# Performance work log

Measured on AMD Instinct MI355X. Metric: run time of the kernel, lower is better.

## Reference

```python
import jax, jax.numpy as jnp
import numpy as np

EPS = 1e-6
BETA = 0.25
COMMIT_W = 1.0


def setup_inputs() -> dict:
    key = jax.random.key(0)
    k1, k2, k3 = jax.random.split(key, 3)
    b, c, h, w = 8, 256, 32, 32
    n_e, e_dim = 16384, 256
    z = jax.random.normal(k1, (b, c, h, w), jnp.float32)
    # frozen_codebook = randn(n_e, e_dim) * e_dim**-0.5
    codebook = jax.random.normal(k2, (n_e, e_dim), jnp.float32) * (e_dim ** -0.5)
    # nn.Linear(e_dim, in_channels, bias=False) weight: (in_channels, e_dim)
    W = jax.random.normal(k3, (c, e_dim), jnp.float32) * (e_dim ** -0.5)
    return {"z": z, "codebook": codebook, "W": W}


def _rotate_to(src, tgt):
    # Rotation trick (Fifty et al.): rotate src onto tgt direction with a
    # detached Householder-style transform; gradient flows through src only.
    # src, tgt: (n, d)
    norm_src = jnp.linalg.norm(src, axis=-1, keepdims=True)
    norm_tgt = jnp.linalg.norm(tgt, axis=-1, keepdims=True)
    u = src / (norm_src + EPS)
    q = tgt / (norm_tgt + EPS)
    uq = u + q
    w_ = jax.lax.stop_gradient(uq / (jnp.linalg.norm(uq, axis=-1, keepdims=True) + EPS))
    u_d = jax.lax.stop_gradient(u)
    q_d = jax.lax.stop_gradient(q)
    rot = (src
           - 2.0 * jnp.sum(src * w_, axis=-1, keepdims=True) * w_
           + 2.0 * jnp.sum(src * u_d, axis=-1, keepdims=True) * q_d)
    return rot * jax.lax.stop_gradient(norm_tgt / (norm_src + EPS))


def reference(z, codebook, W):
    b, c, h, w = z.shape
    # b c h w -> (b*h*w, c)
    z_flat = jnp.transpose(z, (0, 2, 3, 1)).reshape(-1, c)
    # implicit codebook: frozen codes through linear projection
    emb = codebook @ W.T  # (n_e, c)
    # squared L2 distances (no grad needed for argmin)
    d = (jnp.sum(z_flat ** 2, axis=1, keepdims=True)
         + jnp.sum(emb ** 2, axis=1)
         - 2.0 * (z_flat @ emb.T))  # (n_tok, n_e)
    indices = jnp.argmin(d, axis=1)  # (n_tok,)
    z_q_flat = emb[indices]  # gather quantized vectors
    loss = COMMIT_W * (jnp.mean((jax.lax.stop_gradient(z_flat) - z_q_flat) ** 2)
                       + BETA * jnp.mean((z_flat - jax.lax.stop_gradient(z_q_flat)) ** 2))
    z_q_flat = _rotate_to(z_flat, z_q_flat)
    z_q = jnp.transpose(z_q_flat.reshape(b, h, w, c), (0, 3, 1, 2))
    return z_q, loss, indices
```

## Files before the change

kernel.cpp:

```cpp
#include <hip/hip_runtime.h>
#include <math.h>

#define EPSV 1e-6f
#define NTOK 8192
#define NE   16384
#define DIM  256

using short8 = __attribute__((ext_vector_type(8))) short;
using f32x4v = __attribute__((ext_vector_type(4))) float;
using f32x16 = __attribute__((ext_vector_type(16))) float;

__device__ __forceinline__ unsigned short f2bf(float v) {
    unsigned int u = __float_as_uint(v);
    u += 0x7fffu + ((u >> 16) & 1u);
    return (unsigned short)(u >> 16);
}
__device__ __forceinline__ float bf2f(unsigned short h) {
    return __uint_as_float(((unsigned int)h) << 16);
}

__device__ __forceinline__ void gload_lds16(const void* g, void* s) {
    __builtin_amdgcn_global_load_lds(
        (const __attribute__((address_space(1))) void*)g,
        (__attribute__((address_space(3))) void*)s, 16, 0, 0);
}

__device__ __forceinline__ void split8(const float4 a, const float4 b,
                                       short8& h, short8& l) {
    float f[8] = {a.x, a.y, a.z, a.w, b.x, b.y, b.z, b.w};
#pragma unroll
    for (int j = 0; j < 8; ++j) {
        unsigned short hh = f2bf(f[j]);
        h[j] = (short)hh;
        l[j] = (short)f2bf(f[j] - bf2f(hh));
    }
}

__global__ __launch_bounds__(256) void k0a_transpose(
    const float* __restrict__ zin, float* __restrict__ z_flat,
    unsigned short* __restrict__ zh, unsigned short* __restrict__ zl) {
    __shared__ float tile[64][65];
    const int tid = threadIdx.x;
    const int yx0 = blockIdx.x * 64, c0 = blockIdx.y * 64, b = blockIdx.z;
    const int sub = tid >> 6, ln = tid & 63;
#pragma unroll
    for (int j = 0; j < 16; ++j) {
        int cl = j * 4 + sub;
        tile[cl][ln] = zin[((size_t)(b * 256 + c0 + cl) << 10) + yx0 + ln];
    }
    __syncthreads();
#pragma unroll
    for (int j = 0; j < 16; ++j) {
        int tl = j * 4 + sub;
        float v = tile[ln][tl];
        size_t o = (size_t)(b * 1024 + yx0 + tl) * 256 + c0 + ln;
        z_flat[o] = v;
        unsigned short h = f2bf(v);
        zh[o] = h;
        zl[o] = f2bf(v - bf2f(h));
    }
}

__global__ __launch_bounds__(256) void k0b_sz(const float* __restrict__ z_flat,
                                              float* __restrict__ sz) {
    const int w = threadIdx.x >> 6, lane = threadIdx.x & 63;
    const int t = blockIdx.x * 4 + w;
    const float4 v = *(const float4*)(z_flat + (size_t)t * 256 + lane * 4);
    double s = (double)v.x * v.x + (double)v.y * v.y + (double)v.z * v.z +
               (double)v.w * v.w;
#pragma unroll
    for (int m = 1; m < 64; m <<= 1) s += __shfl_xor(s, m);
    if (lane == 0) sz[t] = (float)s;
}

__global__ __launch_bounds__(256) void k0pre(const float* __restrict__ Wm,
                                             unsigned short* __restrict__ wh,
                                             unsigned short* __restrict__ wl) {
    const int i = (blockIdx.x * 256 + threadIdx.x) * 4;
    const float4 v = *(const float4*)(Wm + i);
    float f[4] = {v.x, v.y, v.z, v.w};
#pragma unroll
    for (int j = 0; j < 4; ++j) {
        unsigned short h = f2bf(f[j]);
        wh[i + j] = h;
        wl[i + j] = f2bf(f[j] - bf2f(h));
    }
}

__global__ __launch_bounds__(256, 2) void k0c_emb(
    const float* __restrict__ cb, const unsigned short* __restrict__ wh,
    const unsigned short* __restrict__ wl, float* __restrict__ emb,
    unsigned short* __restrict__ eh, unsigned short* __restrict__ el) {
    __shared__ char smemC[65536];
    const int tid = threadIdx.x;
    const int w = tid >> 6, lane = tid & 63;
    const int quad = lane >> 4, lr = lane & 15;
    const int wr = w & 1, wc = w >> 1;
    const int n0 = blockIdx.x * 128, c0 = blockIdx.y * 128;

    f32x4v acc[4][4];
#pragma unroll
    for (int mt = 0; mt < 4; ++mt)
#pragma unroll
        for (int nt = 0; nt < 4; ++nt)
            acc[mt][nt] = (f32x4v){0.f, 0.f, 0.f, 0.f};

    for (int kc = 0; kc < 4; ++kc) {
        __syncthreads();
#pragma unroll
        for (int i = 0; i < 16; ++i) {
            int s = i * 4 + w;
            int u = s * 64 + lane;
            const void* g;
            if (s < 32) {
                int kg = u >> 7, row = u & 127;
                g = cb + (size_t)(n0 + row) * 256 + kc * 64 + kg * 4;
            } else if (s < 48) {
                int u1 = u - 2048;
                int kg = u1 >> 7, row = u1 & 127;
                g = wh + (size_t)(c0 + row) * 256 + kc * 64 + kg * 8;
            } else {
                int u2 = u - 3072;
                int kg = u2 >> 7, row = u2 & 127;
                g = wl + (size_t)(c0 + row) * 256 + kc * 64 + kg * 8;
            }
            gload_lds16(g, smemC + ((size_t)u << 4));
        }
        __syncthreads();
#pragma unroll
        for (int ks = 0; ks < 2; ++ks) {
            short8 Ah[4], Al[4], Bh[4], Bl[4];
#pragma unroll
            for (int mt = 0; mt < 4; ++mt) {
                int m = wr * 64 + mt * 16 + lr;
                int kg2 = ks * 8 + quad * 2;
                float4 f0 = *(const float4*)(smemC + (((size_t)kg2 * 128 + m) << 4));
                float4 f1 = *(const float4*)(smemC + ((((size_t)kg2 + 1) * 128 + m) << 4));
                split8(f0, f1, Ah[mt], Al[mt]);
            }
#pragma unroll
            for (int nt = 0; nt < 4; ++nt) {
                int n = wc * 64 + nt * 16 + lr;
                int ku = (ks * 4 + quad) * 128 + n;
                Bh[nt] = *(const short8*)(smemC + (((size_t)2048 + ku) << 4));
                Bl[nt] = *(const short8*)(smemC + (((size_t)3072 + ku) << 4));
            }
#pragma unroll
            for (int mt = 0; mt < 4; ++mt)
#pragma unroll
                for (int nt = 0; nt < 4; ++nt) {
                    f32x4v a = acc[mt][nt];
                    a = __builtin_amdgcn_mfma_f32_16x16x32_bf16(Ah[mt], Bh[nt], a, 0, 0, 0);
                    a = __builtin_amdgcn_mfma_f32_16x16x32_bf16(Ah[mt], Bl[nt], a, 0, 0, 0);
                    a = __builtin_amdgcn_mfma_f32_16x16x32_bf16(Al[mt], Bh[nt], a, 0, 0, 0);
                    a = __builtin_amdgcn_mfma_f32_16x16x32_bf16(Al[mt], Bl[nt], a, 0, 0, 0);
                    acc[mt][nt] = a;
                }
        }
    }
#pragma unroll
    for (int mt = 0; mt < 4; ++mt)
#pragma unroll
        for (int rr = 0; rr < 4; ++rr) {
            int row = n0 + wr * 64 + mt * 16 + quad * 4 + rr;
#pragma unroll
            for (int nt = 0; nt < 4; ++nt) {
                int col = c0 + wc * 64 + nt * 16 + lr;
                size_t o = (size_t)row * 256 + col;
                float v = acc[mt][nt][rr];
                emb[o] = v;
                unsigned short h = f2bf(v);
                eh[o] = h;
                el[o] = f2bf(v - bf2f(h));
            }
        }
}

__global__ __launch_bounds__(256) void k0d_se(const float* __restrict__ emb,
                                              float* __restrict__ se) {
    const int w = threadIdx.x >> 6, lane = threadIdx.x & 63;
    const int n = blockIdx.x * 4 + w;
    const float4 v = *(const float4*)(emb + (size_t)n * 256 + lane * 4);
    double s = (double)v.x * v.x + (double)v.y * v.y + (double)v.z * v.z +
               (double)v.w * v.w;
#pragma unroll
    for (int m = 1; m < 64; m <<= 1) s += __shfl_xor(s, m);
    if (lane == 0) se[n] = (float)s;
}

__global__ __launch_bounds__(256, 2) void k1_dist_argmin(
    const unsigned short* __restrict__ zh, const unsigned short* __restrict__ zl,
    const unsigned short* __restrict__ eh, const unsigned short* __restrict__ el,
    const float* __restrict__ sz, const float* __restrict__ se,
    float* __restrict__ pval, int* __restrict__ pidx) {
    __shared__ char smem[65536];
    const int tid = threadIdx.x;
    const int w = tid >> 6, lane = tid & 63;
    const int col = lane & 31, half = lane >> 5;
    const int tokBase = blockIdx.x * 128;
    const int rowBase = tokBase + w * 32;
    const int slab = blockIdx.y;
    const int slabBase = slab * 2048;

    short8 Ah[16], Al[16];
#pragma unroll
    for (int ks = 0; ks < 16; ++ks) {
        size_t o = (size_t)(rowBase + col) * 256 + ks * 16 + half * 8;
        Ah[ks] = *(const short8*)(zh + o);
        Al[ks] = *(const short8*)(zl + o);
    }

    float szrow[16];
#pragma unroll
    for (int r = 0; r < 16; ++r)
        szrow[r] = sz[rowBase + (r & 3) + 8 * (r >> 2) + 4 * half];

    float minv[16];
    int mini[16];
#pragma unroll
    for (int r = 0; r < 16; ++r) {
        minv[r] = INFINITY;
        mini[r] = 0;
    }

    const int BASE = col * 512 + ((half ^ (col & 1)) << 4) + ((col & 30) << 4);

    auto stage = [&](int buf, int ch) {
        const int colBase = slabBase + ch * 32;
#pragma unroll
        for (int i = 0; i < 8; ++i) {
            int u = i * 256 + tid;
            int fmt = u >> 10;
            int u1 = u & 1023;
            int c2 = u1 >> 5, kgs = u1 & 31;
            int kg = kgs ^ c2;
            const unsigned short* g =
                (fmt ? el : eh) + (size_t)(colBase + c2) * 256 + kg * 8;
            gload_lds16(g, smem + buf * 32768 + ((size_t)u << 4));
        }
    };

    stage(0, 0);
    __syncthreads();

    for (int ch = 0; ch < 64; ++ch) {
        const int cur = ch & 1;
        if (ch + 1 < 64) stage(cur ^ 1, ch + 1);

        const float sec = se[slabBase + ch * 32 + col];

        f32x16 acc = {};
        const char* sp = smem + cur * 32768;
        const char* spl = sp + 16384;
#pragma unroll
        for (int ks = 0; ks < 16; ++ks) {
            const int a = BASE ^ (ks << 5);
            short8 Bh = *(const short8*)(sp + a);
            short8 Bl = *(const short8*)(spl + a);
            acc = __builtin_amdgcn_mfma_f32_32x32x16_bf16(Ah[ks], Bh, acc, 0, 0, 0);
            acc = __builtin_amdgcn_mfma_f32_32x32x16_bf16(Ah[ks], Bl, acc, 0, 0, 0);
            acc = __builtin_amdgcn_mfma_f32_32x32x16_bf16(Al[ks], Bh, acc, 0, 0, 0);
        }

        const int colg = slabBase + ch * 32 + col;
#pragma unroll
        for (int r = 0; r < 16; ++r) {
            float szse = __fadd_rn(szrow[r], sec);
            float d = fmaf(-2.0f, acc[r], szse);
            if (d < minv[r]) {
                minv[r] = d;
                mini[r] = colg;
            }
        }
        __syncthreads();
    }

#pragma unroll
    for (int st = 1; st < 32; st <<= 1) {
#pragma unroll
        for (int r = 0; r < 16; ++r) {
            float ov = __shfl_xor(minv[r], st);
            int oi = __shfl_xor(mini[r], st);
            if (ov < minv[r] || (ov == minv[r] && oi < mini[r])) {
                minv[r] = ov;
                mini[r] = oi;
            }
        }
    }
    if (col == 0) {
#pragma unroll
        for (int r = 0; r < 16; ++r) {
            int row = rowBase + (r & 3) + 8 * (r >> 2) + 4 * half;
            pval[(size_t)row * 8 + slab] = minv[r];
            pidx[(size_t)row * 8 + slab] = mini[r];
        }
    }
}

__global__ __launch_bounds__(256) void k3a_token(
    const float* __restrict__ z_flat, const float* __restrict__ emb,
    const float* __restrict__ pval, const int* __restrict__ pidx,
    float* __restrict__ alpha, float* __restrict__ beta,
    int* __restrict__ idxf, float* __restrict__ out,
    float* __restrict__ lpart) {
    __shared__ float red[4];
    const int w = threadIdx.x >> 6, lane = threadIdx.x & 63;
    const int t = blockIdx.x * 4 + w;

    float bv = INFINITY;
    int bi = 0x7fffffff;
    if (lane < 8) {
        bv = pval[(size_t)t * 8 + lane];
        bi = pidx[(size_t)t * 8 + lane];
    }
#pragma unroll
    for (int st = 1; st < 8; st <<= 1) {
        float ov = __shfl_xor(bv, st);
        int oi = __shfl_xor(bi, st);
        if (ov < bv || (ov == bv && oi < bi)) { bv = ov; bi = oi; }
    }
    const int best = __shfl(bi, 0);

    const float4 zv = *(const float4*)(z_flat + (size_t)t * 256 + lane * 4);
    const float4 ev = *(const float4*)(emb + (size_t)best * 256 + lane * 4);
    float szs = zv.x * zv.x + zv.y * zv.y + zv.z * zv.z + zv.w * zv.w;
    float ses = ev.x * ev.x + ev.y * ev.y + ev.z * ev.z + ev.w * ev.w;
    float zes = zv.x * ev.x + zv.y * ev.y + zv.z * ev.z + zv.w * ev.w;
    float dx = zv.x - ev.x, dy = zv.y - ev.y, dz = zv.z - ev.z, dw = zv.w - ev.w;
    float sqs = dx * dx + dy * dy + dz * dz + dw * dw;
#pragma unroll
    for (int m = 1; m < 64; m <<= 1) {
        szs += __shfl_xor(szs, m);
        ses += __shfl_xor(ses, m);
        zes += __shfl_xor(zes, m);
        sqs += __shfl_xor(sqs, m);
    }
    if (lane == 0) {
        float ns = sqrtf(szs), nt = sqrtf(ses);
        float inv_s = 1.0f / (ns + EPSV);
        float inv_t = 1.0f / (nt + EPSV);
        float s2 = szs * inv_s;
        float su = szs * inv_s * inv_s;
        float sq = ses * inv_t * inv_t;
        float uq = zes * inv_s * inv_t;
        float nw = sqrtf(su + sq + 2.0f * uq);
        float inv_w = 1.0f / (nw + EPSV);
        float s1 = (s2 + zes * inv_t) * inv_w;
        float scale = nt * inv_s;
        float a = scale * (1.0f - 2.0f * s1 * inv_w * inv_s);
        float bb = scale * inv_t * 2.0f * (s2 - s1 * inv_w);
        alpha[t] = a;
        beta[t] = bb;
        idxf[t] = best;
        out[2097153 + t] = (float)best;
        red[w] = sqs;
    }
    __syncthreads();
    if (threadIdx.x == 0)
        lpart[blockIdx.x] = red[0] + red[1] + red[2] + red[3];
}

__global__ __launch_bounds__(256) void k4_loss(float* __restrict__ out,
                                               const float* __restrict__ lpart) {
    __shared__ float red[4];
    const int tid = threadIdx.x;
    float s = 0.0f;
    for (int i = tid; i < 2048; i += 256) s += lpart[i];
#pragma unroll
    for (int m = 1; m < 64; m <<= 1) s += __shfl_xor(s, m);
    if ((tid & 63) == 0) red[tid >> 6] = s;
    __syncthreads();
    if (tid == 0)
        out[2097152] = 1.25f * (red[0] + red[1] + red[2] + red[3]) *
                       (1.0f / 2097152.0f);
}

__global__ __launch_bounds__(256) void k3b_zq(
    const float* __restrict__ zin, const float* __restrict__ emb,
    const float* __restrict__ alpha, const float* __restrict__ beta,
    const int* __restrict__ idxf, float* __restrict__ out) {
    const int i = blockIdx.x * 256 + threadIdx.x;
    const int c = (i >> 10) & 255;
    const int t = ((i >> 18) << 10) | (i & 1023);
    out[i] = alpha[t] * zin[i] + beta[t] * emb[(size_t)idxf[t] * 256 + c];
}

extern "C" void kernel_launch(void* const* d_in, const int* in_sizes, int n_in,
                              void* d_out, int out_size, void* d_ws,
                              size_t ws_size, hipStream_t stream) {
    (void)in_sizes; (void)n_in; (void)out_size; (void)ws_size;
    const float* zin = (const float*)d_in[0];
    const float* cb  = (const float*)d_in[1];
    const float* Wm  = (const float*)d_in[2];
    float* out = (float*)d_out;
    char* ws = (char*)d_ws;

    float*          z_flat = (float*)(ws + 0);
    unsigned short* zh     = (unsigned short*)(ws + 8388608);
    unsigned short* zl     = (unsigned short*)(ws + 12582912);
    float*          emb    = (float*)(ws + 16777216);
    unsigned short* eh     = (unsigned short*)(ws + 33554432);
    unsigned short* el     = (unsigned short*)(ws + 41943040);
    float*          sz     = (float*)(ws + 50331648);
    float*          se     = (float*)(ws + 50364416);
    float*          pval   = (float*)(ws + 50429952);
    int*            pidx   = (int*)(ws + 50692096);
    float*          alpha  = (float*)(ws + 50954240);
    float*          beta   = (float*)(ws + 50987008);
    int*            idxf   = (int*)(ws + 51019776);
    float*          lpart  = (float*)(ws + 51052544);
    unsigned short* wh     = (unsigned short*)(ws + 51060736);
    unsigned short* wl     = (unsigned short*)(ws + 51191808);

    k0a_transpose<<<dim3(16, 4, 8), 256, 0, stream>>>(zin, z_flat, zh, zl);
    k0b_sz<<<2048, 256, 0, stream>>>(z_flat, sz);
    k0pre<<<64, 256, 0, stream>>>(Wm, wh, wl);
    k0c_emb<<<dim3(128, 2), 256, 0, stream>>>(cb, wh, wl, emb, eh, el);
    k0d_se<<<4096, 256, 0, stream>>>(emb, se);
    k1_dist_argmin<<<dim3(64, 8), 256, 0, stream>>>(zh, zl, eh, el, sz, se,
                                                    pval, pidx);
    k3a_token<<<2048, 256, 0, stream>>>(z_flat, emb, pval, pidx, alpha, beta,
                                        idxf, out, lpart);
    k4_loss<<<1, 256, 0, stream>>>(out, lpart);
    k3b_zq<<<8192, 256, 0, stream>>>(zin, emb, alpha, beta, idxf, out);
}
```

Measured before the change: 309.2 us.

## Fuse token norm into transpose and split MFMA accumulators into three chains

The separate squared-norm kernel is removed. Each transpose block now loops over all channels of its tokens and accumulates the squared norms in double precision, which saves a launch and a re-read of z_flat. In the distance kernel the three bf16-split MFMAs now write to independent accumulators instead of one serial chain, so they can issue back to back without waiting on each other. The cost is more accumulator registers and a different summation order, which can change argmin tie-breaking slightly. The transpose grid also shrinks to 128 blocks, which lowers parallelism for that kernel.

```diff
diff --git a/kernel.cpp b/kernel.cpp
--- a/kernel.cpp
+++ b/kernel.cpp
@@ -38,39 +38,44 @@
 
 __global__ __launch_bounds__(256) void k0a_transpose(
     const float* __restrict__ zin, float* __restrict__ z_flat,
-    unsigned short* __restrict__ zh, unsigned short* __restrict__ zl) {
+    unsigned short* __restrict__ zh, unsigned short* __restrict__ zl,
+    float* __restrict__ sz) {
     __shared__ float tile[64][65];
     const int tid = threadIdx.x;
-    const int yx0 = blockIdx.x * 64, c0 = blockIdx.y * 64, b = blockIdx.z;
+    const int yx0 = blockIdx.x * 64, b = blockIdx.y;
     const int sub = tid >> 6, ln = tid & 63;
+    double dacc[16];
+#pragma unroll
+    for (int j = 0; j < 16; ++j) dacc[j] = 0.0;
+
+    for (int cc = 0; cc < 4; ++cc) {
+        const int c0 = cc * 64;
+        __syncthreads();
+#pragma unroll
+        for (int j = 0; j < 16; ++j) {
+            int cl = j * 4 + sub;
+            tile[cl][ln] = zin[((size_t)(b * 256 + c0 + cl) << 10) + yx0 + ln];
+        }
+        __syncthreads();
+#pragma unroll
+        for (int j = 0; j < 16; ++j) {
+            int tl = j * 4 + sub;
+            float v = tile[ln][tl];
+            size_t o = (size_t)(b * 1024 + yx0 + tl) * 256 + c0 + ln;
+            z_flat[o] = v;
+            unsigned short h = f2bf(v);
+            zh[o] = h;
+            zl[o] = f2bf(v - bf2f(h));
+            dacc[j] += (double)v * v;
+        }
+    }
 #pragma unroll
     for (int j = 0; j < 16; ++j) {
-        int cl = j * 4 + sub;
-        tile[cl][ln] = zin[((size_t)(b * 256 + c0 + cl) << 10) + yx0 + ln];
-    }
-    __syncthreads();
-#pragma unroll
-    for (int j = 0; j < 16; ++j) {
-        int tl = j * 4 + sub;
-        float v = tile[ln][tl];
-        size_t o = (size_t)(b * 1024 + yx0 + tl) * 256 + c0 + ln;
-        z_flat[o] = v;
-        unsigned short h = f2bf(v);
-        zh[o] = h;
-        zl[o] = f2bf(v - bf2f(h));
-    }
-}
-
-__global__ __launch_bounds__(256) void k0b_sz(const float* __restrict__ z_flat,
-                                              float* __restrict__ sz) {
-    const int w = threadIdx.x >> 6, lane = threadIdx.x & 63;
-    const int t = blockIdx.x * 4 + w;
-    const float4 v = *(const float4*)(z_flat + (size_t)t * 256 + lane * 4);
-    double s = (double)v.x * v.x + (double)v.y * v.y + (double)v.z * v.z +
-               (double)v.w * v.w;
-#pragma unroll
-    for (int m = 1; m < 64; m <<= 1) s += __shfl_xor(s, m);
-    if (lane == 0) sz[t] = (float)s;
+        double s = dacc[j];
+#pragma unroll
+        for (int m = 1; m < 64; m <<= 1) s += __shfl_xor(s, m);
+        if (ln == 0) sz[b * 1024 + yx0 + j * 4 + sub] = (float)s;
+    }
 }
 
 __global__ __launch_bounds__(256) void k0pre(const float* __restrict__ Wm,
@@ -249,7 +254,7 @@
 
         const float sec = se[slabBase + ch * 32 + col];
 
-        f32x16 acc = {};
+        f32x16 accA = {}, accB = {}, accC = {};
         const char* sp = smem + cur * 32768;
         const char* spl = sp + 16384;
 #pragma unroll
@@ -257,16 +262,17 @@
             const int a = BASE ^ (ks << 5);
             short8 Bh = *(const short8*)(sp + a);
             short8 Bl = *(const short8*)(spl + a);
-            acc = __builtin_amdgcn_mfma_f32_32x32x16_bf16(Ah[ks], Bh, acc, 0, 0, 0);
-            acc = __builtin_amdgcn_mfma_f32_32x32x16_bf16(Ah[ks], Bl, acc, 0, 0, 0);
-            acc = __builtin_amdgcn_mfma_f32_32x32x16_bf16(Al[ks], Bh, acc, 0, 0, 0);
+            accA = __builtin_amdgcn_mfma_f32_32x32x16_bf16(Ah[ks], Bh, accA, 0, 0, 0);
+            accB = __builtin_amdgcn_mfma_f32_32x32x16_bf16(Ah[ks], Bl, accB, 0, 0, 0);
+            accC = __builtin_amdgcn_mfma_f32_32x32x16_bf16(Al[ks], Bh, accC, 0, 0, 0);
         }
 
         const int colg = slabBase + ch * 32 + col;
 #pragma unroll
         for (int r = 0; r < 16; ++r) {
+            float dot = (accB[r] + accC[r]) + accA[r];
             float szse = __fadd_rn(szrow[r], sec);
-            float d = fmaf(-2.0f, acc[r], szse);
+            float d = fmaf(-2.0f, dot, szse);
             if (d < minv[r]) {
                 minv[r] = d;
                 mini[r] = colg;
@@ -412,8 +418,7 @@
     unsigned short* wh     = (unsigned short*)(ws + 51060736);
     unsigned short* wl     = (unsigned short*)(ws + 51191808);
 
-    k0a_transpose<<<dim3(16, 4, 8), 256, 0, stream>>>(zin, z_flat, zh, zl);
-    k0b_sz<<<2048, 256, 0, stream>>>(z_flat, sz);
+    k0a_transpose<<<dim3(16, 8), 256, 0, stream>>>(zin, z_flat, zh, zl, sz);
     k0pre<<<64, 256, 0, stream>>>(Wm, wh, wl);
     k0c_emb<<<dim3(128, 2), 256, 0, stream>>>(cb, wh, wl, emb, eh, el);
     k0d_se<<<4096, 256, 0, stream>>>(emb, se);
```

Measured after the change: 432.8 us. 40.0% more time.
